# Kernel tuning notes

Hardware: AMD Instinct MI355X
Metric: run time of the kernel (lower is better)

The kernel has to match this reference:

```python
import jax, jax.numpy as jnp
import numpy as np

TEMPERATURE = 0.5


def setup_inputs() -> dict:
    key = jax.random.key(0)
    k1, k2 = jax.random.split(key)
    B, C, H, W = 64, 256, 32, 32
    inputs = jax.random.normal(k1, (B, C, H, W), dtype=jnp.float32)
    targets = jax.random.normal(k2, (B, C, H, W), dtype=jnp.float32)
    return {"inputs": inputs, "targets": targets}


def reference(inputs, targets):
    # [B, C, H, W] -> [H, W, B, C]
    x = jnp.transpose(inputs, (2, 3, 0, 1))
    y = jnp.transpose(targets, (2, 3, 0, 1))
    B = x.shape[-2]
    feats = jnp.concatenate([x, y], axis=-2)  # [H, W, 2B, C]
    eps = jnp.finfo(feats.dtype).eps
    # cosine similarity: normalize each vector with eps-clamped norm, then dot
    norms = jnp.maximum(jnp.linalg.norm(feats, axis=-1, keepdims=True), eps)
    fn = feats / norms
    sim = jnp.einsum('hwic,hwjc->hwij', fn, fn)  # [H, W, 2B, 2B]
    # mask self-similarity diagonal with -inf
    mask = jnp.eye(2 * B, dtype=bool)
    sim = jnp.where(mask, -jnp.inf, sim)
    log_sm = jax.nn.log_softmax(sim / TEMPERATURE, axis=-1)
    pos = jnp.concatenate(
        [jnp.diagonal(log_sm, offset=B, axis1=-2, axis2=-1),
         jnp.diagonal(log_sm, offset=-B, axis1=-2, axis2=-1)],
        axis=-1,
    )  # [H, W, 2B]
    return -jnp.mean(pos)
```

## Files before the change

### kernel.cpp

```cpp
#include <hip/hip_runtime.h>
#include <stdint.h>

#define HWPOS 1024
#define CCH   256
#define RROWS 128
#define EPSF  1.1920928955078125e-07f

typedef __attribute__((ext_vector_type(8))) short   short8;
typedef __attribute__((ext_vector_type(4))) float   float4v;

__device__ __forceinline__ unsigned short f2bf(float f) {
  uint32_t x = __float_as_uint(f);
  x += 0x7FFFu + ((x >> 16) & 1u);
  return (unsigned short)(x >> 16);
}


__global__ __launch_bounds__(256) void k_transpose(const float* __restrict__ inp,
                                                   const float* __restrict__ tgt,
                                                   unsigned short* __restrict__ wsF) {
  const int t   = threadIdx.x;
  const int j   = t & 7;
  const int h4  = (t >> 3) & 7;
  const int g   = t >> 6;
  const int rr  = blockIdx.y;
  const int hw0 = blockIdx.x * 32;
  const int m   = rr & 7;
  const int slot = g * 8 + j;
  const int c8   = g * 8 + (j ^ m);
  const int q4   = slot >> 3;
  const int s8   = slot & 7;
  const size_t coff = (size_t)c8 * 8 * HWPOS + hw0 + h4 * 4;
  const float* p0 = inp + (size_t)rr * CCH * HWPOS + coff;
  const float* p1 = tgt + (size_t)rr * CCH * HWPOS + coff;
  float4 v0[8], v1[8];
#pragma unroll
  for (int e = 0; e < 8; ++e) v0[e] = *(const float4*)(p0 + (size_t)e * HWPOS);
#pragma unroll
  for (int e = 0; e < 8; ++e) v1[e] = *(const float4*)(p1 + (size_t)e * HWPOS);
#pragma unroll
  for (int rsel = 0; rsel < 2; ++rsel) {
    const int r = rsel ? (rr + 64) : rr;
    float4* v = rsel ? v1 : v0;
#pragma unroll
    for (int qq = 0; qq < 4; ++qq) {
      float s0 = (qq == 0) ? v[0].x : (qq == 1) ? v[0].y : (qq == 2) ? v[0].z : v[0].w;
      float s1 = (qq == 0) ? v[1].x : (qq == 1) ? v[1].y : (qq == 2) ? v[1].z : v[1].w;
      float s2 = (qq == 0) ? v[2].x : (qq == 1) ? v[2].y : (qq == 2) ? v[2].z : v[2].w;
      float s3 = (qq == 0) ? v[3].x : (qq == 1) ? v[3].y : (qq == 2) ? v[3].z : v[3].w;
      float s4 = (qq == 0) ? v[4].x : (qq == 1) ? v[4].y : (qq == 2) ? v[4].z : v[4].w;
      float s5 = (qq == 0) ? v[5].x : (qq == 1) ? v[5].y : (qq == 2) ? v[5].z : v[5].w;
      float s6 = (qq == 0) ? v[6].x : (qq == 1) ? v[6].y : (qq == 2) ? v[6].z : v[6].w;
      float s7 = (qq == 0) ? v[7].x : (qq == 1) ? v[7].y : (qq == 2) ? v[7].z : v[7].w;
      uint4 o;
      o.x = f2bf(s0) | ((uint32_t)f2bf(s1) << 16);
      o.y = f2bf(s2) | ((uint32_t)f2bf(s3) << 16);
      o.z = f2bf(s4) | ((uint32_t)f2bf(s5) << 16);
      o.w = f2bf(s6) | ((uint32_t)f2bf(s7) << 16);
      const size_t a16 = (size_t)(hw0 + h4 * 4 + qq) * 4096 + (size_t)q4 * 1024 + r * 8 + s8;
      *(uint4*)(wsF + a16 * 8) = o;
    }
  }
}

__global__ __launch_bounds__(512, 4) void k_gram(const unsigned short* __restrict__ wsF,
                                                 float* __restrict__ out) {
  __shared__ unsigned short Fs[2][8192];
  __shared__ float sInv[RROWS];
  __shared__ float wred[8];
  const int t  = threadIdx.x;
  const int hw = blockIdx.x;
  const int lane = t & 63;
  const int w    = t >> 6;
  const int lid  = lane & 15;
  const int quad = lane >> 4;
  const int lm   = lid & 7;
  float4v acc[8];
#pragma unroll
  for (int ni = 0; ni < 8; ++ni) acc[ni] = (float4v){0.f, 0.f, 0.f, 0.f};
  const unsigned short* gsrc = wsF + (size_t)hw * 65536;
#pragma unroll
  for (int it = 0; it < 2; ++it) {
    const size_t ch = (size_t)it * 512 + t;
    __builtin_amdgcn_global_load_lds(
        (const __attribute__((address_space(1))) unsigned int*)(gsrc + ch * 8),
        (__attribute__((address_space(3))) unsigned int*)(&Fs[0][0] + ch * 8),
        16, 0, 0);
  }
  __syncthreads();
#pragma unroll
  for (int q = 0; q < 4; ++q) {
    if (q < 3) {
#pragma unroll
      for (int it = 0; it < 2; ++it) {
        const size_t ch = (size_t)it * 512 + t;
        __builtin_amdgcn_global_load_lds(
            (const __attribute__((address_space(1))) unsigned int*)(gsrc + (size_t)(q + 1) * 16384 + ch * 8),
            (__attribute__((address_space(3))) unsigned int*)(&Fs[(q + 1) & 1][0] + ch * 8),
            16, 0, 0);
      }
    }
    const unsigned short* B = &Fs[q & 1][0];
#pragma unroll
    for (int ks2 = 0; ks2 < 2; ++ks2) {
      const int off = (((ks2 * 4 + quad) ^ lm) << 3);
      short8 a = *(const short8*)&B[((w << 4) | lid) * 64 + off];
#pragma unroll
      for (int ni = 0; ni < 8; ++ni) {
        short8 b = *(const short8*)&B[((ni << 4) | lid) * 64 + off];
        acc[ni] = __builtin_amdgcn_mfma_f32_16x16x32_bf16(a, b, acc[ni], 0, 0, 0);
      }
    }
    __syncthreads();
  }
  {
    float diagv = 0.f;
#pragma unroll
    for (int ni = 0; ni < 8; ++ni) {
      if (ni == w) {
#pragma unroll
        for (int e = 0; e < 4; ++e)
          if (e == (lid & 3)) diagv = acc[ni][e];
      }
    }
    if ((lid >> 2) == quad) {
      sInv[(w << 4) | lid] = 1.0f / fmaxf(sqrtf(diagv), EPSF);
    }
  }
  __syncthreads();
  float invj[8];
#pragma unroll
  for (int ni = 0; ni < 8; ++ni) invj[ni] = sInv[(ni << 4) | lid];
  const int tj = (w + 4) & 7;
  float lacc = 0.f;
#pragma unroll
  for (int reg = 0; reg < 4; ++reg) {
    const int rloc = quad * 4 + reg;
    const int rg   = (w << 4) | rloc;
    const float invi = sInv[rg];
    float v[8];
#pragma unroll
    for (int ni = 0; ni < 8; ++ni) v[ni] = 2.0f * acc[ni][reg] * invi * invj[ni];
#pragma unroll
    for (int ni = 0; ni < 8; ++ni)
      if (ni == w && lid == rloc) v[ni] = -3.0e38f;
    float mx = v[0];
#pragma unroll
    for (int ni = 1; ni < 8; ++ni) mx = fmaxf(mx, v[ni]);
#pragma unroll
    for (int s = 1; s < 16; s <<= 1) mx = fmaxf(mx, __shfl_xor(mx, s, 16));
    float sm = 0.f;
#pragma unroll
    for (int ni = 0; ni < 8; ++ni) sm += __expf(v[ni] - mx);
#pragma unroll
    for (int s = 1; s < 16; s <<= 1) sm += __shfl_xor(sm, s, 16);
    const float lse = mx + __logf(sm);
    float cand = 0.f;
#pragma unroll
    for (int ni = 0; ni < 8; ++ni)
      if (ni == tj) cand = v[ni];
    const float vp = __shfl(cand, rloc, 16);
    lacc += vp - lse;
  }
#pragma unroll
  for (int s = 1; s < 64; s <<= 1) lacc += __shfl_xor(lacc, s, 64);
  if (lane == 0) wred[w] = lacc;
  __syncthreads();
  if (t == 0) {
    float tot = 0.f;
#pragma unroll
    for (int i = 0; i < 8; ++i) tot += wred[i];
    atomicAdd(out, -tot * (1.0f / 2097152.0f));
  }
}

__global__ void k_zero(float* __restrict__ out) { out[0] = 0.0f; }

extern "C" void kernel_launch(void* const* d_in, const int* in_sizes, int n_in,
                              void* d_out, int out_size, void* d_ws, size_t ws_size,
                              hipStream_t stream) {
  const float* inp = (const float*)d_in[0];
  const float* tgt = (const float*)d_in[1];
  unsigned short* wsF = (unsigned short*)d_ws;
  k_zero<<<1, 1, 0, stream>>>((float*)d_out);
  k_transpose<<<dim3(32, 64), 256, 0, stream>>>(inp, tgt, wsF);
  k_gram<<<dim3(HWPOS), 512, 0, stream>>>(wsF, (float*)d_out);
}
```

Baseline: 186.1 us.

## Stage transpose through swizzled LDS tile for coalesced bf16 workspace writes

Rewrites the fp32-to-bf16 transpose kernel to load a 4-row x 64-channel x 64-position tile into registers, convert and write it into an XOR-swizzled shared-memory buffer, then read it back so each thread emits full 16-byte chunks in the gram kernel's layout. Previously each thread wrote scattered 16-byte chunks directly to global memory with poor write coalescing. The grid changes to 16x32x4 blocks. This adds an LDS round trip and a barrier, and must reproduce the same chunk swizzle the gram kernel expects.

Result: no change. 188.3 us (+1.2%).

```diff
diff --git a/kernel.cpp b/kernel.cpp
--- a/kernel.cpp
+++ b/kernel.cpp
@@ -19,47 +19,56 @@
 __global__ __launch_bounds__(256) void k_transpose(const float* __restrict__ inp,
                                                    const float* __restrict__ tgt,
                                                    unsigned short* __restrict__ wsF) {
+  __shared__ unsigned short L[4 * 64 * 64];
   const int t   = threadIdx.x;
-  const int j   = t & 7;
-  const int h4  = (t >> 3) & 7;
-  const int g   = t >> 6;
-  const int rr  = blockIdx.y;
-  const int hw0 = blockIdx.x * 32;
-  const int m   = rr & 7;
-  const int slot = g * 8 + j;
-  const int c8   = g * 8 + (j ^ m);
-  const int q4   = slot >> 3;
-  const int s8   = slot & 7;
-  const size_t coff = (size_t)c8 * 8 * HWPOS + hw0 + h4 * 4;
-  const float* p0 = inp + (size_t)rr * CCH * HWPOS + coff;
-  const float* p1 = tgt + (size_t)rr * CCH * HWPOS + coff;
-  float4 v0[8], v1[8];
+  const int hwg = blockIdx.x;
+  const int rg  = blockIdx.y;
+  const int cqz = blockIdx.z;
+  const int hw0 = hwg * 64;
+  const int rbase = rg * 4;
+  const float* src = (rg < 16) ? (inp + (size_t)(rg * 4) * CCH * HWPOS)
+                               : (tgt + (size_t)((rg - 16) * 4) * CCH * HWPOS);
+  const int hw16 = t & 15;
+  const int cs   = t >> 4;
+  const int cbase = cqz * 64 + cs * 4;
+  float4 v[4][4];
 #pragma unroll
-  for (int e = 0; e < 8; ++e) v0[e] = *(const float4*)(p0 + (size_t)e * HWPOS);
+  for (int rl = 0; rl < 4; ++rl)
 #pragma unroll
-  for (int e = 0; e < 8; ++e) v1[e] = *(const float4*)(p1 + (size_t)e * HWPOS);
+    for (int cc = 0; cc < 4; ++cc)
+      v[rl][cc] = *(const float4*)(src + ((size_t)rl * CCH + cbase + cc) * HWPOS
+                                   + hw0 + hw16 * 4);
+  const int c8l  = cs >> 1;
+  const int half = (cs & 1) * 4;
 #pragma unroll
-  for (int rsel = 0; rsel < 2; ++rsel) {
-    const int r = rsel ? (rr + 64) : rr;
-    float4* v = rsel ? v1 : v0;
+  for (int rl = 0; rl < 4; ++rl) {
 #pragma unroll
-    for (int qq = 0; qq < 4; ++qq) {
-      float s0 = (qq == 0) ? v[0].x : (qq == 1) ? v[0].y : (qq == 2) ? v[0].z : v[0].w;
-      float s1 = (qq == 0) ? v[1].x : (qq == 1) ? v[1].y : (qq == 2) ? v[1].z : v[1].w;
-      float s2 = (qq == 0) ? v[2].x : (qq == 1) ? v[2].y : (qq == 2) ? v[2].z : v[2].w;
-      float s3 = (qq == 0) ? v[3].x : (qq == 1) ? v[3].y : (qq == 2) ? v[3].z : v[3].w;
-      float s4 = (qq == 0) ? v[4].x : (qq == 1) ? v[4].y : (qq == 2) ? v[4].z : v[4].w;
-      float s5 = (qq == 0) ? v[5].x : (qq == 1) ? v[5].y : (qq == 2) ? v[5].z : v[5].w;
-      float s6 = (qq == 0) ? v[6].x : (qq == 1) ? v[6].y : (qq == 2) ? v[6].z : v[6].w;
-      float s7 = (qq == 0) ? v[7].x : (qq == 1) ? v[7].y : (qq == 2) ? v[7].z : v[7].w;
-      uint4 o;
-      o.x = f2bf(s0) | ((uint32_t)f2bf(s1) << 16);
-      o.y = f2bf(s2) | ((uint32_t)f2bf(s3) << 16);
-      o.z = f2bf(s4) | ((uint32_t)f2bf(s5) << 16);
-      o.w = f2bf(s6) | ((uint32_t)f2bf(s7) << 16);
-      const size_t a16 = (size_t)(hw0 + h4 * 4 + qq) * 4096 + (size_t)q4 * 1024 + r * 8 + s8;
-      *(uint4*)(wsF + a16 * 8) = o;
+    for (int e = 0; e < 4; ++e) {
+      const int hwl = hw16 * 4 + e;
+      const int k   = c8l ^ ((hwl >> 3) & 7);
+      float a = (e == 0) ? v[rl][0].x : (e == 1) ? v[rl][0].y : (e == 2) ? v[rl][0].z : v[rl][0].w;
+      float b = (e == 0) ? v[rl][1].x : (e == 1) ? v[rl][1].y : (e == 2) ? v[rl][1].z : v[rl][1].w;
+      float c = (e == 0) ? v[rl][2].x : (e == 1) ? v[rl][2].y : (e == 2) ? v[rl][2].z : v[rl][2].w;
+      float d = (e == 0) ? v[rl][3].x : (e == 1) ? v[rl][3].y : (e == 2) ? v[rl][3].z : v[rl][3].w;
+      uint2 o;
+      o.x = f2bf(a) | ((uint32_t)f2bf(b) << 16);
+      o.y = f2bf(c) | ((uint32_t)f2bf(d) << 16);
+      *(uint2*)&L[((rl * 64 + hwl) * 8 + k) * 8 + half] = o;
     }
+  }
+  __syncthreads();
+  const int s8  = t & 7;
+  const int rl2 = (t >> 3) & 3;
+  const int hwp = t >> 5;
+  const int rglob = rbase + rl2;
+  const int c8w = s8 ^ (rglob & 7);
+#pragma unroll
+  for (int li = 0; li < 8; ++li) {
+    const int hwl = li * 8 + hwp;
+    const int k   = c8w ^ ((hwl >> 3) & 7);
+    uint4 d = *(const uint4*)&L[((rl2 * 64 + hwl) * 8 + k) * 8];
+    const size_t a16 = (size_t)(hw0 + hwl) * 4096 + (size_t)cqz * 1024 + rglob * 8 + s8;
+    *(uint4*)(wsF + a16 * 8) = d;
   }
 }
 
@@ -183,6 +192,6 @@
   const float* tgt = (const float*)d_in[1];
   unsigned short* wsF = (unsigned short*)d_ws;
   k_zero<<<1, 1, 0, stream>>>((float*)d_out);
-  k_transpose<<<dim3(32, 64), 256, 0, stream>>>(inp, tgt, wsF);
+  k_transpose<<<dim3(16, 32, 4), 256, 0, stream>>>(inp, tgt, wsF);
   k_gram<<<dim3(HWPOS), 512, 0, stream>>>(wsF, (float*)d_out);
 }
```

## Store normalized-gram operands as FP8 and use FP8 MFMA with single-shot LDS load

Applied to the files above, without the earlier changes.

The transpose kernel now packs features into FP8 (e4m3) instead of bf16 and uses a new 16-byte swizzled layout. This halves the intermediate workspace traffic that is written and then read back. The gram kernel loads the whole 32KB per-position tile into LDS in one shot instead of a double-buffered pipeline, and uses fp8 16x16x32 MFMA. The separate zeroing kernel is folded into the transpose kernel. The trade-off is much lower input precision for the similarity, which could change the loss beyond tolerance.

After: 173.9 us. 6.5% less time.

```diff
diff --git a/kernel.cpp b/kernel.cpp
--- a/kernel.cpp
+++ b/kernel.cpp
@@ -6,66 +6,54 @@
 #define RROWS 128
 #define EPSF  1.1920928955078125e-07f
 
-typedef __attribute__((ext_vector_type(8))) short   short8;
-typedef __attribute__((ext_vector_type(4))) float   float4v;
+typedef __attribute__((ext_vector_type(4))) float float4v;
 
-__device__ __forceinline__ unsigned short f2bf(float f) {
-  uint32_t x = __float_as_uint(f);
-  x += 0x7FFFu + ((x >> 16) & 1u);
-  return (unsigned short)(x >> 16);
+__device__ __forceinline__ uint32_t pk4_fp8(float a, float b, float c, float d) {
+  int v = 0;
+  v = __builtin_amdgcn_cvt_pk_fp8_f32(a, b, v, false);
+  v = __builtin_amdgcn_cvt_pk_fp8_f32(c, d, v, true);
+  return (uint32_t)v;
 }
 
 
 __global__ __launch_bounds__(256) void k_transpose(const float* __restrict__ inp,
                                                    const float* __restrict__ tgt,
-                                                   unsigned short* __restrict__ wsF) {
-  const int t   = threadIdx.x;
-  const int j   = t & 7;
-  const int h4  = (t >> 3) & 7;
-  const int g   = t >> 6;
-  const int rr  = blockIdx.y;
-  const int hw0 = blockIdx.x * 32;
-  const int m   = rr & 7;
-  const int slot = g * 8 + j;
-  const int c8   = g * 8 + (j ^ m);
-  const int q4   = slot >> 3;
-  const int s8   = slot & 7;
-  const size_t coff = (size_t)c8 * 8 * HWPOS + hw0 + h4 * 4;
-  const float* p0 = inp + (size_t)rr * CCH * HWPOS + coff;
-  const float* p1 = tgt + (size_t)rr * CCH * HWPOS + coff;
-  float4 v0[8], v1[8];
+                                                   unsigned char* __restrict__ wsF,
+                                                   float* __restrict__ out) {
+  const int t    = threadIdx.x;
+  const int hq   = t & 7;
+  const int dd   = (t >> 3) & 15;
+  const int rsel = t >> 7;
+  const int r    = blockIdx.y * 2 + rsel;
+  const int hw0  = blockIdx.x * 32;
+  if (blockIdx.x == 0 && blockIdx.y == 0 && t == 0) out[0] = 0.0f;
+  const int m = r & 15;
+  const int s = dd ^ m;
+  const float* src = (r < 64) ? (inp + (size_t)r * CCH * HWPOS)
+                              : (tgt + (size_t)(r - 64) * CCH * HWPOS);
+  const float* p = src + (size_t)(dd * 16) * HWPOS + hw0 + hq * 4;
+  float4 v[16];
 #pragma unroll
-  for (int e = 0; e < 8; ++e) v0[e] = *(const float4*)(p0 + (size_t)e * HWPOS);
+  for (int e = 0; e < 16; ++e) v[e] = *(const float4*)(p + (size_t)e * HWPOS);
 #pragma unroll
-  for (int e = 0; e < 8; ++e) v1[e] = *(const float4*)(p1 + (size_t)e * HWPOS);
+  for (int q = 0; q < 4; ++q) {
+    float x[16];
 #pragma unroll
-  for (int rsel = 0; rsel < 2; ++rsel) {
-    const int r = rsel ? (rr + 64) : rr;
-    float4* v = rsel ? v1 : v0;
-#pragma unroll
-    for (int qq = 0; qq < 4; ++qq) {
-      float s0 = (qq == 0) ? v[0].x : (qq == 1) ? v[0].y : (qq == 2) ? v[0].z : v[0].w;
-      float s1 = (qq == 0) ? v[1].x : (qq == 1) ? v[1].y : (qq == 2) ? v[1].z : v[1].w;
-      float s2 = (qq == 0) ? v[2].x : (qq == 1) ? v[2].y : (qq == 2) ? v[2].z : v[2].w;
-      float s3 = (qq == 0) ? v[3].x : (qq == 1) ? v[3].y : (qq == 2) ? v[3].z : v[3].w;
-      float s4 = (qq == 0) ? v[4].x : (qq == 1) ? v[4].y : (qq == 2) ? v[4].z : v[4].w;
-      float s5 = (qq == 0) ? v[5].x : (qq == 1) ? v[5].y : (qq == 2) ? v[5].z : v[5].w;
-      float s6 = (qq == 0) ? v[6].x : (qq == 1) ? v[6].y : (qq == 2) ? v[6].z : v[6].w;
-      float s7 = (qq == 0) ? v[7].x : (qq == 1) ? v[7].y : (qq == 2) ? v[7].z : v[7].w;
-      uint4 o;
-      o.x = f2bf(s0) | ((uint32_t)f2bf(s1) << 16);
-      o.y = f2bf(s2) | ((uint32_t)f2bf(s3) << 16);
-      o.z = f2bf(s4) | ((uint32_t)f2bf(s5) << 16);
-      o.w = f2bf(s6) | ((uint32_t)f2bf(s7) << 16);
-      const size_t a16 = (size_t)(hw0 + h4 * 4 + qq) * 4096 + (size_t)q4 * 1024 + r * 8 + s8;
-      *(uint4*)(wsF + a16 * 8) = o;
-    }
+    for (int e = 0; e < 16; ++e)
+      x[e] = (q == 0) ? v[e].x : (q == 1) ? v[e].y : (q == 2) ? v[e].z : v[e].w;
+    uint4 o;
+    o.x = pk4_fp8(x[0],  x[1],  x[2],  x[3]);
+    o.y = pk4_fp8(x[4],  x[5],  x[6],  x[7]);
+    o.z = pk4_fp8(x[8],  x[9],  x[10], x[11]);
+    o.w = pk4_fp8(x[12], x[13], x[14], x[15]);
+    const size_t a = (size_t)(hw0 + hq * 4 + q) * 32768 + (size_t)r * 256 + s * 16;
+    *(uint4*)(wsF + a) = o;
   }
 }
 
-__global__ __launch_bounds__(512, 4) void k_gram(const unsigned short* __restrict__ wsF,
+__global__ __launch_bounds__(512, 4) void k_gram(const unsigned char* __restrict__ wsF,
                                                  float* __restrict__ out) {
-  __shared__ unsigned short Fs[2][8192];
+  __shared__ unsigned char Fs[32768];
   __shared__ float sInv[RROWS];
   __shared__ float wred[8];
   const int t  = threadIdx.x;
@@ -74,44 +62,30 @@
   const int w    = t >> 6;
   const int lid  = lane & 15;
   const int quad = lane >> 4;
-  const int lm   = lid & 7;
   float4v acc[8];
 #pragma unroll
   for (int ni = 0; ni < 8; ++ni) acc[ni] = (float4v){0.f, 0.f, 0.f, 0.f};
-  const unsigned short* gsrc = wsF + (size_t)hw * 65536;
+  const unsigned char* gsrc = wsF + (size_t)hw * 32768;
 #pragma unroll
-  for (int it = 0; it < 2; ++it) {
+  for (int it = 0; it < 4; ++it) {
     const size_t ch = (size_t)it * 512 + t;
     __builtin_amdgcn_global_load_lds(
-        (const __attribute__((address_space(1))) unsigned int*)(gsrc + ch * 8),
-        (__attribute__((address_space(3))) unsigned int*)(&Fs[0][0] + ch * 8),
+        (const __attribute__((address_space(1))) unsigned int*)(gsrc + ch * 16),
+        (__attribute__((address_space(3))) unsigned int*)(Fs + ch * 16),
         16, 0, 0);
   }
   __syncthreads();
+  const int rowA = (w << 4) | lid;
 #pragma unroll
-  for (int q = 0; q < 4; ++q) {
-    if (q < 3) {
+  for (int ks = 0; ks < 8; ++ks) {
+    const int d    = 2 * ks + (quad >> 1);
+    const int off  = ((d ^ lid) << 4) + (quad & 1) * 8;
+    long a = *(const long*)&Fs[rowA * 256 + off];
 #pragma unroll
-      for (int it = 0; it < 2; ++it) {
-        const size_t ch = (size_t)it * 512 + t;
-        __builtin_amdgcn_global_load_lds(
-            (const __attribute__((address_space(1))) unsigned int*)(gsrc + (size_t)(q + 1) * 16384 + ch * 8),
-            (__attribute__((address_space(3))) unsigned int*)(&Fs[(q + 1) & 1][0] + ch * 8),
-            16, 0, 0);
-      }
+    for (int ni = 0; ni < 8; ++ni) {
+      long b = *(const long*)&Fs[(((ni << 4) | lid)) * 256 + off];
+      acc[ni] = __builtin_amdgcn_mfma_f32_16x16x32_fp8_fp8(a, b, acc[ni], 0, 0, 0);
     }
-    const unsigned short* B = &Fs[q & 1][0];
-#pragma unroll
-    for (int ks2 = 0; ks2 < 2; ++ks2) {
-      const int off = (((ks2 * 4 + quad) ^ lm) << 3);
-      short8 a = *(const short8*)&B[((w << 4) | lid) * 64 + off];
-#pragma unroll
-      for (int ni = 0; ni < 8; ++ni) {
-        short8 b = *(const short8*)&B[((ni << 4) | lid) * 64 + off];
-        acc[ni] = __builtin_amdgcn_mfma_f32_16x16x32_bf16(a, b, acc[ni], 0, 0, 0);
-      }
-    }
-    __syncthreads();
   }
   {
     float diagv = 0.f;
@@ -148,12 +122,12 @@
 #pragma unroll
     for (int ni = 1; ni < 8; ++ni) mx = fmaxf(mx, v[ni]);
 #pragma unroll
-    for (int s = 1; s < 16; s <<= 1) mx = fmaxf(mx, __shfl_xor(mx, s, 16));
+    for (int sh = 1; sh < 16; sh <<= 1) mx = fmaxf(mx, __shfl_xor(mx, sh, 16));
     float sm = 0.f;
 #pragma unroll
     for (int ni = 0; ni < 8; ++ni) sm += __expf(v[ni] - mx);
 #pragma unroll
-    for (int s = 1; s < 16; s <<= 1) sm += __shfl_xor(sm, s, 16);
+    for (int sh = 1; sh < 16; sh <<= 1) sm += __shfl_xor(sm, sh, 16);
     const float lse = mx + __logf(sm);
     float cand = 0.f;
 #pragma unroll
@@ -163,7 +137,7 @@
     lacc += vp - lse;
   }
 #pragma unroll
-  for (int s = 1; s < 64; s <<= 1) lacc += __shfl_xor(lacc, s, 64);
+  for (int sh = 1; sh < 64; sh <<= 1) lacc += __shfl_xor(lacc, sh, 64);
   if (lane == 0) wred[w] = lacc;
   __syncthreads();
   if (t == 0) {
@@ -174,15 +148,12 @@
   }
 }
 
-__global__ void k_zero(float* __restrict__ out) { out[0] = 0.0f; }
-
 extern "C" void kernel_launch(void* const* d_in, const int* in_sizes, int n_in,
                               void* d_out, int out_size, void* d_ws, size_t ws_size,
                               hipStream_t stream) {
   const float* inp = (const float*)d_in[0];
   const float* tgt = (const float*)d_in[1];
-  unsigned short* wsF = (unsigned short*)d_ws;
-  k_zero<<<1, 1, 0, stream>>>((float*)d_out);
-  k_transpose<<<dim3(32, 64), 256, 0, stream>>>(inp, tgt, wsF);
+  unsigned char* wsF = (unsigned char*)d_ws;
+  k_transpose<<<dim3(32, 64), 256, 0, stream>>>(inp, tgt, wsF, (float*)d_out);
   k_gram<<<dim3(HWPOS), 512, 0, stream>>>(wsF, (float*)d_out);
 }
```
